# Kernel optimization log

Hardware: AMD Instinct MI355X
Metric: run time of the kernel (lower is better)

The kernel has to match this reference:

```python
import jax, jax.numpy as jnp
import numpy as np

N = 200000   # active voxels
G = 128      # dense grid extent per axis
C = 128      # hidden channels
IN_C = 1
TEMB = 6
K = 27       # 3x3x3 kernel offsets


def _build_neighbors():
    # Sample N unique voxel coordinates in a G^3 grid and build the 27-offset
    # rulebook: neighbor_idx[k, i] = index of voxel at coord[i] + offset[k],
    # or N (sentinel -> zero-padded feature row) if inactive.
    rng = np.random.default_rng(0)
    lin = np.sort(rng.choice(G ** 3, size=N, replace=False)).astype(np.int64)
    x, r = lin // (G * G), lin % (G * G)
    y, z = r // G, r % G
    nidx = np.full((K, N), N, dtype=np.int32)
    k = 0
    for dx in (-1, 0, 1):
        for dy in (-1, 0, 1):
            for dz in (-1, 0, 1):
                nx, ny, nz = x + dx, y + dy, z + dz
                valid = (nx >= 0) & (nx < G) & (ny >= 0) & (ny < G) & (nz >= 0) & (nz < G)
                key = nx * (G * G) + ny * G + nz
                pos = np.searchsorted(lin, key)
                posc = np.clip(pos, 0, N - 1)
                found = valid & (lin[posc] == key)
                nidx[k] = np.where(found, posc, N).astype(np.int32)
                k += 1
    return jnp.asarray(nidx)


def setup_inputs() -> dict:
    key = jax.random.key(0)
    ks = jax.random.split(key, 8)
    s = jnp.float32(0.05)
    return {
        "features": jax.random.normal(ks[0], (N, IN_C), jnp.float32),
        "t": jax.random.randint(ks[1], (N,), 0, 1000, jnp.int32),
        "neighbor_idx": _build_neighbors(),
        "W1": jax.random.normal(ks[2], (K, IN_C + TEMB, C), jnp.float32) * s,
        "b1": jnp.zeros((C,), jnp.float32),
        "W2": jax.random.normal(ks[3], (K, C, C), jnp.float32) * s,
        "b2": jnp.zeros((C,), jnp.float32),
        "W3": jax.random.normal(ks[4], (C, C), jnp.float32) * s,
        "b3": jnp.zeros((C,), jnp.float32),
        "W4": jax.random.normal(ks[5], (C, 1), jnp.float32) * s,
        "b4": jnp.zeros((1,), jnp.float32),
    }


def _sinusoidal(t, dim):
    half = dim // 2
    freqs = (2.0 ** jnp.arange(half, dtype=jnp.float32)) * jnp.pi  # 2^k * pi
    ang = t.astype(jnp.float32)[:, None] * freqs[None, :]
    return jnp.concatenate([jnp.sin(ang), jnp.cos(ang)], -1)  # [N, dim]


def _sparse_conv3(x, W, b, nidx):
    # Submanifold sparse 3x3x3 conv: for each of 27 offsets, gather neighbor
    # features (zero row for missing) and accumulate a [Cin,Cout] matmul.
    xpad = jnp.concatenate([x, jnp.zeros((1, x.shape[1]), x.dtype)], 0)  # sentinel row
    acc0 = jnp.zeros((x.shape[0], W.shape[-1]), x.dtype)

    def step(acc, kw):
        idx, Wk = kw
        return acc + xpad[idx] @ Wk, None

    acc, _ = jax.lax.scan(step, acc0, (nidx, W))
    return acc + b


def reference(features, t, neighbor_idx, W1, b1, W2, b2, W3, b3, W4, b4):
    # time-embedding concat  [N, 1+6]
    x = jnp.concatenate([features, _sinusoidal(t, TEMB)], -1)
    # SparseConv3d(k=3) + Dropout(eval: identity) + SiLU
    h = jax.nn.silu(_sparse_conv3(x, W1, b1, neighbor_idx))
    h = jax.nn.silu(_sparse_conv3(h, W2, b2, neighbor_idx))
    # SparseConv3d(k=1) + SiLU  == pointwise matmul
    h = jax.nn.silu(h @ W3 + b3)
    # final 1x1 conv to out_channels=1
    return h @ W4 + b4
```

## Files before the change

### kernel.cpp

```cpp
#include <hip/hip_runtime.h>
#include <math.h>

#define N_VOX 200000
#define CCH   128
#define KOFF  27

typedef __attribute__((ext_vector_type(8))) short bf16x8;
typedef __attribute__((ext_vector_type(4))) float f32x4;

__device__ __forceinline__ float silu_f(float x) {
    return x / (1.0f + expf(-x));
}
__device__ __forceinline__ unsigned short f2bf(float x) {
    unsigned int u = __float_as_uint(x);
    u = (u + 0x7FFFu + ((u >> 16) & 1u)) >> 16;
    return (unsigned short)u;
}
__device__ __forceinline__ int xcd_swz(int orig, int nwg) {
    int q = nwg >> 3, r = nwg & 7;
    int xcd = orig & 7, pos = orig >> 3;
    return (xcd < r ? xcd * (q + 1) : r * (q + 1) + (xcd - r) * q) + pos;
}
__device__ __forceinline__ void gload_lds16(const void* g, void* l) {
    __builtin_amdgcn_global_load_lds(
        (const __attribute__((address_space(1))) unsigned int*)g,
        (__attribute__((address_space(3))) unsigned int*)l, 16, 0, 0);
}

__global__ void embed_kernel(const float* __restrict__ feat,
                             const int* __restrict__ t,
                             unsigned short* __restrict__ xeb) {
    int i = blockIdx.x * blockDim.x + threadIdx.x;
    if (i > N_VOX) return;
    union { unsigned short u[8]; int4 v; } o;
    if (i == N_VOX) {
        o.v = make_int4(0, 0, 0, 0);
    } else {
        o.u[0] = f2bf(feat[i]);
        float tf = (float)t[i];
#pragma unroll
        for (int kk = 0; kk < 3; ++kk) {
            float freq = (float)M_PI * (float)(1 << kk);
            float ang = tf * freq;
            o.u[1 + kk] = f2bf(sinf(ang));
            o.u[4 + kk] = f2bf(cosf(ang));
        }
        o.u[7] = 0;
    }
    *(int4*)(xeb + (size_t)i * 8) = o.v;
}

__global__ void convert_w1(const float* __restrict__ W1,
                           unsigned short* __restrict__ W1f) {
    int g = blockIdx.x * 256 + threadIdx.x;
    if (g >= 7 * 8 * 64) return;
    int l = g & 63;
    int rest = g >> 6;
    int nf = rest & 7;
    int kk = rest >> 3;
    int o = kk * 4 + (l >> 4);
    int co = nf * 16 + (l & 15);
    union { unsigned short u[8]; int4 v; } out;
#pragma unroll
    for (int j = 0; j < 8; ++j) {
        float w = 0.f;
        if (o < KOFF && j < 7) w = W1[((size_t)o * 7 + j) * CCH + co];
        out.u[j] = f2bf(w);
    }
    *(int4*)(W1f + (size_t)g * 8) = out.v;
}

__global__ void convert_w2(const float* __restrict__ W2,
                           unsigned short* __restrict__ W2f) {
    int g = blockIdx.x * 256 + threadIdx.x;
    int l = g & 63;
    int rest = g >> 6;
    int nf = rest & 7;
    int kkk = rest >> 3;
    int k = kkk >> 2, kk = kkk & 3;
    int ci0 = kk * 32 + (l >> 4) * 8;
    int co = nf * 16 + (l & 15);
    union { unsigned short u[8]; int4 v; } out;
#pragma unroll
    for (int j = 0; j < 8; ++j)
        out.u[j] = f2bf(W2[((size_t)k * CCH + ci0 + j) * CCH + co]);
    *(int4*)(W2f + (size_t)g * 8) = out.v;
}

__global__ void convert_w3(const float* __restrict__ W3,
                           unsigned short* __restrict__ W3f) {
    int g = blockIdx.x * 256 + threadIdx.x;
    if (g >= 4 * 8 * 64) return;
    int l = g & 63;
    int rest = g >> 6;
    int nf = rest & 7;
    int kk = rest >> 3;
    int ci0 = kk * 32 + (l >> 4) * 8;
    int co = nf * 16 + (l & 15);
    union { unsigned short u[8]; int4 v; } out;
#pragma unroll
    for (int j = 0; j < 8; ++j)
        out.u[j] = f2bf(W3[(size_t)(ci0 + j) * CCH + co]);
    *(int4*)(W3f + (size_t)g * 8) = out.v;
}

__global__ __launch_bounds__(256) void conv1_mfma(
    const unsigned short* __restrict__ xeb, const int* __restrict__ nidx,
    const unsigned short* __restrict__ W1f, const float* __restrict__ b1,
    unsigned short* __restrict__ h1b) {
    __shared__ int4 bufmem[2048];
    __shared__ int idxAll[128 * 28];

    int tid = threadIdx.x;
    int l = tid & 63, w = tid >> 6;
    int mw = w >> 1, nwv = w & 1;
    int wg = xcd_swz(blockIdx.x, gridDim.x);
    int v0 = wg * 128;

    for (int g = tid; g < KOFF * 128; g += 256) {
        int k = g >> 7, vi = g & 127;
        int v = v0 + vi;
        idxAll[vi * 28 + k] = (v < N_VOX) ? nidx[(size_t)k * N_VOX + v] : N_VOX;
    }
    if (tid < 128) idxAll[tid * 28 + 27] = N_VOX;
    __syncthreads();

    f32x4 acc[4][4];
#pragma unroll
    for (int m = 0; m < 4; ++m)
#pragma unroll
        for (int n = 0; n < 4; ++n) acc[m][n] = (f32x4)0.f;

    {
        int4 g0[2]; int rr[2], cc[2];
#pragma unroll
        for (int u = 0; u < 2; ++u) {
            int q = u * 256 + tid;
            int r = q >> 2, oo = q & 3;
            int idx = idxAll[r * 28 + oo];
            g0[u] = *(const int4*)(xeb + (size_t)idx * 8);
            rr[u] = r; cc[u] = oo ^ (r & 3);
        }
#pragma unroll
        for (int u = 0; u < 2; ++u) bufmem[rr[u] * 5 + cc[u]] = g0[u];
    }
    __syncthreads();

    for (int kk = 0; kk < 7; ++kk) {
        int cur = kk & 1;
        int4 gg[2]; int rr[2], cc[2];
        if (kk < 6) {
#pragma unroll
            for (int u = 0; u < 2; ++u) {
                int q = u * 256 + tid;
                int r = q >> 2, oo = q & 3;
                int idx = idxAll[r * 28 + (kk + 1) * 4 + oo];
                gg[u] = *(const int4*)(xeb + (size_t)idx * 8);
                rr[u] = r; cc[u] = oo ^ (r & 3);
            }
        }
        bf16x8 a[4], b[4];
#pragma unroll
        for (int n = 0; n < 4; ++n) {
            int nf = nwv * 4 + n;
            b[n] = *(const bf16x8*)(W1f + ((size_t)(kk * 8 + nf) * 64 + l) * 8);
        }
#pragma unroll
        for (int m = 0; m < 4; ++m) {
            int r = mw * 64 + m * 16 + (l & 15);
            int c = l >> 4;
            a[m] = *(const bf16x8*)&bufmem[cur * 640 + r * 5 + (c ^ (r & 3))];
        }
#pragma unroll
        for (int m = 0; m < 4; ++m)
#pragma unroll
            for (int n = 0; n < 4; ++n)
                acc[m][n] = __builtin_amdgcn_mfma_f32_16x16x32_bf16(
                    a[m], b[n], acc[m][n], 0, 0, 0);
        if (kk < 6) {
#pragma unroll
            for (int u = 0; u < 2; ++u)
                bufmem[(cur ^ 1) * 640 + rr[u] * 5 + cc[u]] = gg[u];
        }
        __syncthreads();
    }

    float bias[4];
#pragma unroll
    for (int n = 0; n < 4; ++n) bias[n] = b1[nwv * 64 + n * 16 + (l & 15)];
    unsigned short* H16 = (unsigned short*)bufmem;
#pragma unroll
    for (int m = 0; m < 4; ++m) {
        int rbase = mw * 64 + m * 16 + (l >> 4) * 4;
#pragma unroll
        for (int n = 0; n < 4; ++n) {
            int ch = nwv * 64 + n * 16 + (l & 15);
            int c = ch >> 3;
            f32x4 d = acc[m][n];
#pragma unroll
            for (int ri = 0; ri < 4; ++ri) {
                int r = rbase + ri;
                int s = (c & 8) | ((c & 7) ^ (r & 7));
                H16[r * 128 + s * 8 + (ch & 7)] = f2bf(silu_f(d[ri] + bias[n]));
            }
        }
    }
    __syncthreads();
#pragma unroll
    for (int u = 0; u < 8; ++u) {
        int q = u * 256 + tid;
        int r = q >> 4, s = q & 15;
        int c = (s & 8) | ((s & 7) ^ (r & 7));
        int v = v0 + r;
        if (v < N_VOX)
            *(int4*)(h1b + (size_t)v * CCH + c * 8) = bufmem[r * 16 + s];
    }
    if (blockIdx.x == 0 && tid < 16)
        *(int4*)(h1b + (size_t)N_VOX * CCH + tid * 8) = make_int4(0, 0, 0, 0);
}

#define STAGE_S(buf, sq, ib) {                                             \
    _Pragma("unroll") for (int _u = 0; _u < 8; ++_u) {                     \
        int _q = _u * 256 + tid;                                           \
        int _row = ((_q >> 7) << 4) | (_q & 15);                           \
        int _hi = (_q >> 4) & 3;                                           \
        int _kk = (_q >> 6) & 1;                                           \
        int _idx = idxbuf[ib][_row];                                       \
        gload_lds16((const char*)h1b + ((size_t)(unsigned)_idx << 8) +     \
                        ((sq) & 1) * 128 + _kk * 64 + _hi * 16,            \
                    (void*)&Abuf[buf][_q]);                                \
    }                                                                      \
}

#define LOADB_S(dst, sq) {                                                 \
    const unsigned short* _wb = W2f + (size_t)((sq) >> 1) * 16384 +        \
                                (size_t)((sq) & 1) * 2 * 4096;             \
    _Pragma("unroll") for (int _kk = 0; _kk < 2; ++_kk)                    \
        _Pragma("unroll") for (int _n = 0; _n < 4; ++_n)                   \
            dst[_kk][_n] = *(const bf16x8*)(_wb +                          \
                ((size_t)(_kk * 8 + nwv * 4 + _n) * 64 + l) * 8);          \
}

#define MFMA_S(cur, bfr) {                                                 \
    _Pragma("unroll") for (int _kk = 0; _kk < 2; ++_kk) {                  \
        bf16x8 _a[8];                                                      \
        _Pragma("unroll") for (int _m = 0; _m < 8; ++_m) {                 \
            int _R = mw * 8 + _m;                                          \
            _a[_m] = *(const bf16x8*)&Abuf[cur][((_R * 2 + _kk) << 6) + l];\
        }                                                                  \
        __builtin_amdgcn_s_setprio(1);                                     \
        _Pragma("unroll") for (int _m = 0; _m < 8; ++_m)                   \
            _Pragma("unroll") for (int _n = 0; _n < 4; ++_n)               \
                acc[_m][_n] = __builtin_amdgcn_mfma_f32_16x16x32_bf16(     \
                    _a[_m], bfr[_kk][_n], acc[_m][_n], 0, 0, 0);           \
        __builtin_amdgcn_s_setprio(0);                                     \
    }                                                                      \
}

#define STEP_S(SQ, CUR, DO_STAGE, DO_IDX) {                                \
    bf16x8 bfr[2][4];                                                      \
    LOADB_S(bfr, SQ);                                                      \
    __builtin_amdgcn_sched_barrier(0);                                     \
    if (DO_STAGE) { STAGE_S((CUR) ^ 1, (SQ) + 1, ((((SQ) + 1) >> 1) & 1)); }\
    if (DO_IDX) {                                                          \
        int _k1 = ((SQ) >> 1) + 1;                                         \
        int _v = v0 + tid;                                                 \
        idxbuf[_k1 & 1][tid] =                                             \
            (_v < N_VOX) ? nidx[(size_t)_k1 * N_VOX + _v] : N_VOX;         \
    }                                                                      \
    __builtin_amdgcn_sched_barrier(0);                                     \
    MFMA_S(CUR, bfr);                                                      \
    asm volatile("s_waitcnt vmcnt(0)" ::: "memory");                       \
    __builtin_amdgcn_s_barrier();                                          \
}

__global__ __launch_bounds__(256, 2) void conv2_mfma(
    const unsigned short* __restrict__ h1b, const int* __restrict__ nidx,
    const unsigned short* __restrict__ W2f, const float* __restrict__ b2,
    const unsigned short* __restrict__ W3f, const float* __restrict__ b3,
    const float* __restrict__ W4, const float* __restrict__ b4,
    float* __restrict__ out) {
    __shared__ int4 Abuf[2][2048];
    __shared__ int idxbuf[2][256];
    __shared__ float Osum[512];

    int tid = threadIdx.x;
    int l = tid & 63, w = tid >> 6;
    int mw = w >> 1, nwv = w & 1;
    int wg = xcd_swz(blockIdx.x, gridDim.x);
    int v0 = wg * 256;

    f32x4 acc[8][4];
#pragma unroll
    for (int m = 0; m < 8; ++m)
#pragma unroll
        for (int n = 0; n < 4; ++n) acc[m][n] = (f32x4)0.f;

    {
        int v = v0 + tid;
        idxbuf[0][tid] = (v < N_VOX) ? nidx[v] : N_VOX;
    }
    __syncthreads();
    STAGE_S(0, 0, 0);
    {
        int v = v0 + tid;
        idxbuf[1][tid] = (v < N_VOX) ? nidx[(size_t)N_VOX + v] : N_VOX;
    }
    asm volatile("s_waitcnt vmcnt(0)" ::: "memory");
    __syncthreads();

    for (int sp = 0; sp < 52; sp += 2) {
        STEP_S(sp, 0, true, ((sp >> 1) + 1 < KOFF));
        STEP_S(sp + 1, 1, true, false);
    }
    STEP_S(52, 0, true, false);
    STEP_S(53, 1, false, false);

    float bias2[4];
#pragma unroll
    for (int n = 0; n < 4; ++n) bias2[n] = b2[nwv * 64 + n * 16 + (l & 15)];
    unsigned short* H16 = (unsigned short*)&Abuf[0][0];
#pragma unroll
    for (int m = 0; m < 8; ++m) {
        int rbase = mw * 128 + m * 16 + (l >> 4) * 4;
#pragma unroll
        for (int n = 0; n < 4; ++n) {
            int ch = nwv * 64 + n * 16 + (l & 15);
            int c = ch >> 3;
            f32x4 d = acc[m][n];
#pragma unroll
            for (int ri = 0; ri < 4; ++ri) {
                int r = rbase + ri;
                int s = (c & 8) | ((c & 7) ^ (r & 7));
                H16[r * 128 + s * 8 + (ch & 7)] = f2bf(silu_f(d[ri] + bias2[n]));
            }
        }
    }
    __syncthreads();

    f32x4 p[8][4];
#pragma unroll
    for (int m = 0; m < 8; ++m)
#pragma unroll
        for (int n = 0; n < 4; ++n) p[m][n] = (f32x4)0.f;
#pragma unroll
    for (int kk = 0; kk < 4; ++kk) {
        bf16x8 a[8], b[4];
#pragma unroll
        for (int n = 0; n < 4; ++n) {
            int nf = nwv * 4 + n;
            b[n] = *(const bf16x8*)(W3f + ((size_t)(kk * 8 + nf) * 64 + l) * 8);
        }
#pragma unroll
        for (int m = 0; m < 8; ++m) {
            int r = mw * 128 + m * 16 + (l & 15);
            int c = kk * 4 + (l >> 4);
            int s = (c & 8) | ((c & 7) ^ (r & 7));
            a[m] = *(const bf16x8*)&H16[r * 128 + s * 8];
        }
#pragma unroll
        for (int m = 0; m < 8; ++m)
#pragma unroll
            for (int n = 0; n < 4; ++n)
                p[m][n] = __builtin_amdgcn_mfma_f32_16x16x32_bf16(
                    a[m], b[n], p[m][n], 0, 0, 0);
    }

    float w4v[4], b3v[4];
#pragma unroll
    for (int n = 0; n < 4; ++n) {
        int ch = nwv * 64 + n * 16 + (l & 15);
        w4v[n] = W4[ch];
        b3v[n] = b3[ch];
    }
#pragma unroll
    for (int m = 0; m < 8; ++m) {
        float po[4] = {0.f, 0.f, 0.f, 0.f};
#pragma unroll
        for (int n = 0; n < 4; ++n) {
            f32x4 d = p[m][n];
#pragma unroll
            for (int ri = 0; ri < 4; ++ri)
                po[ri] += silu_f(d[ri] + b3v[n]) * w4v[n];
        }
#pragma unroll
        for (int off = 1; off < 16; off <<= 1)
#pragma unroll
            for (int ri = 0; ri < 4; ++ri)
                po[ri] += __shfl_xor(po[ri], off, 64);
        if ((l & 15) == 0) {
            int rbase = mw * 128 + m * 16 + (l >> 4) * 4;
#pragma unroll
            for (int ri = 0; ri < 4; ++ri)
                Osum[nwv * 256 + rbase + ri] = po[ri];
        }
    }
    __syncthreads();
    {
        int v = v0 + tid;
        if (v < N_VOX) out[v] = Osum[tid] + Osum[256 + tid] + b4[0];
    }
}

extern "C" void kernel_launch(void* const* d_in, const int* in_sizes, int n_in,
                              void* d_out, int out_size, void* d_ws,
                              size_t ws_size, hipStream_t stream) {
    const float* feat = (const float*)d_in[0];
    const int* t      = (const int*)d_in[1];
    const int* nidx   = (const int*)d_in[2];
    const float* W1   = (const float*)d_in[3];
    const float* b1   = (const float*)d_in[4];
    const float* W2   = (const float*)d_in[5];
    const float* b2   = (const float*)d_in[6];
    const float* W3   = (const float*)d_in[7];
    const float* b3   = (const float*)d_in[8];
    const float* W4   = (const float*)d_in[9];
    const float* b4   = (const float*)d_in[10];
    float* out = (float*)d_out;

    char* ws = (char*)d_ws;
    size_t off = 0;
    unsigned short* xeb = (unsigned short*)(ws + off);
    off += ((size_t)(N_VOX + 1) * 8 * 2 + 255) & ~(size_t)255;
    unsigned short* h1b = (unsigned short*)(ws + off);
    off += ((size_t)(N_VOX + 1) * CCH * 2 + 255) & ~(size_t)255;
    unsigned short* W1f = (unsigned short*)(ws + off);
    off += ((size_t)7 * 8 * 64 * 8 * 2 + 255) & ~(size_t)255;
    unsigned short* W2f = (unsigned short*)(ws + off);
    off += ((size_t)(KOFF + 1) * 4 * 8 * 64 * 8 * 2 + 255) & ~(size_t)255;
    unsigned short* W3f = (unsigned short*)(ws + off);

    int grid1 = (N_VOX + 127) / 128;
    int grid2 = (N_VOX + 255) / 256;
    embed_kernel<<<(N_VOX + 1 + 255) / 256, 256, 0, stream>>>(feat, t, xeb);
    convert_w1<<<(7 * 8 * 64 + 255) / 256, 256, 0, stream>>>(W1, W1f);
    convert_w2<<<(KOFF * 4 * 8 * 64) / 256, 256, 0, stream>>>(W2, W2f);
    convert_w3<<<(4 * 8 * 64 + 255) / 256, 256, 0, stream>>>(W3, W3f);
    conv1_mfma<<<grid1, 256, 0, stream>>>(xeb, nidx, W1f, b1, h1b);
    conv2_mfma<<<grid2, 256, 0, stream>>>(h1b, nidx, W2f, b2, W3f, b3, W4, b4, out);
}
```

Measured before the change: 277.3 us.

## Restructure conv2 into 512-thread triple-buffered pipeline with LDS-staged weights

conv2 now runs 512 threads per block (8 waves, 2x4 warp tiling) and uses three LDS buffers holding both gathered activations and W2 slices. Loads go straight to LDS, and each K-half is split into four phases that interleave async gathers with MFMA groups under fine-grained barriers and partial vmcnt waits. Neighbor indices are prefetched into a three-slot ring. The epilogue is reworked so each wave computes a 32-row slice of the W3/W4 head and writes the output directly, with no cross-wave LDS reduction. This is meant to hide gather latency and cut redundant per-wave global weight loads, at the cost of one block per CU and many more barriers.

```diff
diff --git a/kernel.cpp b/kernel.cpp
--- a/kernel.cpp
+++ b/kernel.cpp
@@ -219,113 +219,150 @@
         *(int4*)(h1b + (size_t)N_VOX * CCH + tid * 8) = make_int4(0, 0, 0, 0);
 }
 
-#define STAGE_S(buf, sq, ib) {                                             \
-    _Pragma("unroll") for (int _u = 0; _u < 8; ++_u) {                     \
-        int _q = _u * 256 + tid;                                           \
-        int _row = ((_q >> 7) << 4) | (_q & 15);                           \
-        int _hi = (_q >> 4) & 3;                                           \
-        int _kk = (_q >> 6) & 1;                                           \
-        int _idx = idxbuf[ib][_row];                                       \
-        gload_lds16((const char*)h1b + ((size_t)(unsigned)_idx << 8) +     \
-                        ((sq) & 1) * 128 + _kk * 64 + _hi * 16,            \
-                    (void*)&Abuf[buf][_q]);                                \
-    }                                                                      \
-}
-
-#define LOADB_S(dst, sq) {                                                 \
-    const unsigned short* _wb = W2f + (size_t)((sq) >> 1) * 16384 +        \
-                                (size_t)((sq) & 1) * 2 * 4096;             \
-    _Pragma("unroll") for (int _kk = 0; _kk < 2; ++_kk)                    \
-        _Pragma("unroll") for (int _n = 0; _n < 4; ++_n)                   \
-            dst[_kk][_n] = *(const bf16x8*)(_wb +                          \
-                ((size_t)(_kk * 8 + nwv * 4 + _n) * 64 + l) * 8);          \
-}
-
-#define MFMA_S(cur, bfr) {                                                 \
-    _Pragma("unroll") for (int _kk = 0; _kk < 2; ++_kk) {                  \
-        bf16x8 _a[8];                                                      \
-        _Pragma("unroll") for (int _m = 0; _m < 8; ++_m) {                 \
-            int _R = mw * 8 + _m;                                          \
-            _a[_m] = *(const bf16x8*)&Abuf[cur][((_R * 2 + _kk) << 6) + l];\
-        }                                                                  \
-        __builtin_amdgcn_s_setprio(1);                                     \
-        _Pragma("unroll") for (int _m = 0; _m < 8; ++_m)                   \
-            _Pragma("unroll") for (int _n = 0; _n < 4; ++_n)               \
-                acc[_m][_n] = __builtin_amdgcn_mfma_f32_16x16x32_bf16(     \
-                    _a[_m], bfr[_kk][_n], acc[_m][_n], 0, 0, 0);           \
-        __builtin_amdgcn_s_setprio(0);                                     \
-    }                                                                      \
-}
-
-#define STEP_S(SQ, CUR, DO_STAGE, DO_IDX) {                                \
-    bf16x8 bfr[2][4];                                                      \
-    LOADB_S(bfr, SQ);                                                      \
+#define STG_A(P, s3, h, U) {                                               \
+    int _T = (U) * 8 + w;                                                  \
+    int _r16 = _T >> 1, _kkq = _T & 1;                                     \
+    int _idx = idxL[s3][_r16 * 16 + (l & 15)];                             \
+    gload_lds16((const char*)h1b + ((size_t)(unsigned)_idx << 8) +         \
+                    (h) * 128 + _kkq * 64 + (l >> 4) * 16,                 \
+                (void*)&(P)[(U) * 512 + tid]);                             \
+}
+#define STG_B(P, k2, h, U) {                                               \
+    gload_lds16((const char*)W2f + (size_t)(k2) * 32768 + (h) * 16384 +    \
+                    (size_t)((U) * 512 + tid) * 16,                        \
+                (void*)&(P)[2048 + (U) * 512 + tid]);                      \
+}
+
+#define MFMA8(Q) {                                                         \
+    __builtin_amdgcn_s_setprio(1);                                         \
+    acc[(Q)*2+0][0] = __builtin_amdgcn_mfma_f32_16x16x32_bf16(_a00, bfr[0][0], acc[(Q)*2+0][0], 0, 0, 0); \
+    acc[(Q)*2+0][1] = __builtin_amdgcn_mfma_f32_16x16x32_bf16(_a00, bfr[0][1], acc[(Q)*2+0][1], 0, 0, 0); \
+    acc[(Q)*2+1][0] = __builtin_amdgcn_mfma_f32_16x16x32_bf16(_a10, bfr[0][0], acc[(Q)*2+1][0], 0, 0, 0); \
+    acc[(Q)*2+1][1] = __builtin_amdgcn_mfma_f32_16x16x32_bf16(_a10, bfr[0][1], acc[(Q)*2+1][1], 0, 0, 0); \
+    acc[(Q)*2+0][0] = __builtin_amdgcn_mfma_f32_16x16x32_bf16(_a01, bfr[1][0], acc[(Q)*2+0][0], 0, 0, 0); \
+    acc[(Q)*2+0][1] = __builtin_amdgcn_mfma_f32_16x16x32_bf16(_a01, bfr[1][1], acc[(Q)*2+0][1], 0, 0, 0); \
+    acc[(Q)*2+1][0] = __builtin_amdgcn_mfma_f32_16x16x32_bf16(_a11, bfr[1][0], acc[(Q)*2+1][0], 0, 0, 0); \
+    acc[(Q)*2+1][1] = __builtin_amdgcn_mfma_f32_16x16x32_bf16(_a11, bfr[1][1], acc[(Q)*2+1][1], 0, 0, 0); \
+    __builtin_amdgcn_s_setprio(0);                                         \
+}
+
+#define AREADS(Pc, Q)                                                      \
+    bf16x8 _a00 = *(const bf16x8*)&(Pc)[((mw * 8 + (Q)*2 + 0) * 2 + 0) * 64 + l]; \
+    bf16x8 _a01 = *(const bf16x8*)&(Pc)[((mw * 8 + (Q)*2 + 0) * 2 + 1) * 64 + l]; \
+    bf16x8 _a10 = *(const bf16x8*)&(Pc)[((mw * 8 + (Q)*2 + 1) * 2 + 0) * 64 + l]; \
+    bf16x8 _a11 = *(const bf16x8*)&(Pc)[((mw * 8 + (Q)*2 + 1) * 2 + 1) * 64 + l];
+
+#define PHASE(Pc, Q, STAGE_STMTS) {                                        \
+    AREADS(Pc, Q)                                                          \
+    STAGE_STMTS                                                            \
+    asm volatile("s_barrier" ::: "memory");                                \
+    asm volatile("s_waitcnt lgkmcnt(0)" ::: "memory");                     \
     __builtin_amdgcn_sched_barrier(0);                                     \
-    if (DO_STAGE) { STAGE_S((CUR) ^ 1, (SQ) + 1, ((((SQ) + 1) >> 1) & 1)); }\
-    if (DO_IDX) {                                                          \
-        int _k1 = ((SQ) >> 1) + 1;                                         \
-        int _v = v0 + tid;                                                 \
-        idxbuf[_k1 & 1][tid] =                                             \
-            (_v < N_VOX) ? nidx[(size_t)_k1 * N_VOX + _v] : N_VOX;         \
-    }                                                                      \
+    MFMA8(Q)                                                               \
+    asm volatile("s_barrier" ::: "memory");                                \
+}
+
+#define PHASE_END(Pc, Q, ENDSTMTS) {                                       \
+    AREADS(Pc, Q)                                                          \
+    asm volatile("s_barrier" ::: "memory");                                \
+    asm volatile("s_waitcnt lgkmcnt(0)" ::: "memory");                     \
     __builtin_amdgcn_sched_barrier(0);                                     \
-    MFMA_S(CUR, bfr);                                                      \
-    asm volatile("s_waitcnt vmcnt(0)" ::: "memory");                       \
-    __builtin_amdgcn_s_barrier();                                          \
-}
-
-__global__ __launch_bounds__(256, 2) void conv2_mfma(
+    MFMA8(Q)                                                               \
+    ENDSTMTS                                                               \
+    asm volatile("s_barrier" ::: "memory");                                \
+}
+
+#define RDB(Pc) {                                                          \
+    bfr[0][0] = *(const bf16x8*)&(Pc)[2048 + (0 * 8 + nwv * 2 + 0) * 64 + l]; \
+    bfr[0][1] = *(const bf16x8*)&(Pc)[2048 + (0 * 8 + nwv * 2 + 1) * 64 + l]; \
+    bfr[1][0] = *(const bf16x8*)&(Pc)[2048 + (1 * 8 + nwv * 2 + 0) * 64 + l]; \
+    bfr[1][1] = *(const bf16x8*)&(Pc)[2048 + (1 * 8 + nwv * 2 + 1) * 64 + l]; \
+}
+
+__global__ __launch_bounds__(512, 1) void conv2_mfma(
     const unsigned short* __restrict__ h1b, const int* __restrict__ nidx,
     const unsigned short* __restrict__ W2f, const float* __restrict__ b2,
     const unsigned short* __restrict__ W3f, const float* __restrict__ b3,
     const float* __restrict__ W4, const float* __restrict__ b4,
     float* __restrict__ out) {
-    __shared__ int4 Abuf[2][2048];
-    __shared__ int idxbuf[2][256];
-    __shared__ float Osum[512];
+    __shared__ int4 Pbuf[3][3072];
+    __shared__ int idxL[3][256];
 
     int tid = threadIdx.x;
     int l = tid & 63, w = tid >> 6;
-    int mw = w >> 1, nwv = w & 1;
+    int mw = w >> 2, nwv = w & 3;
     int wg = xcd_swz(blockIdx.x, gridDim.x);
     int v0 = wg * 256;
 
-    f32x4 acc[8][4];
+    for (int g = tid; g < 3 * 256; g += 512) {
+        int k = g >> 8, vi = g & 255;
+        int v = v0 + vi;
+        idxL[k][vi] = (v < N_VOX) ? nidx[(size_t)k * N_VOX + v] : N_VOX;
+    }
+    __syncthreads();
+
+    f32x4 acc[8][2];
 #pragma unroll
     for (int m = 0; m < 8; ++m)
 #pragma unroll
-        for (int n = 0; n < 4; ++n) acc[m][n] = (f32x4)0.f;
-
-    {
-        int v = v0 + tid;
-        idxbuf[0][tid] = (v < N_VOX) ? nidx[v] : N_VOX;
-    }
-    __syncthreads();
-    STAGE_S(0, 0, 0);
-    {
-        int v = v0 + tid;
-        idxbuf[1][tid] = (v < N_VOX) ? nidx[(size_t)N_VOX + v] : N_VOX;
-    }
+        for (int n = 0; n < 2; ++n) acc[m][n] = (f32x4)0.f;
+
+    int4* P0 = Pbuf[0];
+    int4* P1 = Pbuf[1];
+    int4* P2 = Pbuf[2];
+
+    STG_A(P0, 0, 0, 0); STG_A(P0, 0, 0, 1); STG_A(P0, 0, 0, 2); STG_A(P0, 0, 0, 3);
+    STG_B(P0, 0, 0, 0); STG_B(P0, 0, 0, 1);
+    STG_A(P1, 0, 1, 0); STG_A(P1, 0, 1, 1); STG_A(P1, 0, 1, 2); STG_A(P1, 0, 1, 3);
+    STG_B(P1, 0, 1, 0); STG_B(P1, 0, 1, 1);
     asm volatile("s_waitcnt vmcnt(0)" ::: "memory");
     __syncthreads();
 
-    for (int sp = 0; sp < 52; sp += 2) {
-        STEP_S(sp, 0, true, ((sp >> 1) + 1 < KOFF));
-        STEP_S(sp + 1, 1, true, false);
-    }
-    STEP_S(52, 0, true, false);
-    STEP_S(53, 1, false, false);
-
-    float bias2[4];
-#pragma unroll
-    for (int n = 0; n < 4; ++n) bias2[n] = b2[nwv * 64 + n * 16 + (l & 15)];
-    unsigned short* H16 = (unsigned short*)&Abuf[0][0];
+    for (int tp = 0; tp < 27; ++tp) {
+        int s3 = (tp + 1) % 3;
+        int k2 = tp + 1;
+        int knew = tp + 2; if (knew > 26) knew = 26;
+        int slotw = (tp + 2) % 3;
+        int idxreg;
+        {
+            bf16x8 bfr[2][2];
+            RDB(P0);
+            PHASE(P0, 0, {
+                idxreg = nidx[(size_t)knew * N_VOX + v0 + (tid & 255)];
+                STG_A(P2, s3, 0, 0); STG_A(P2, s3, 0, 1);
+            });
+            PHASE(P0, 1, { STG_A(P2, s3, 0, 2); STG_A(P2, s3, 0, 3); });
+            PHASE(P0, 2, { STG_B(P2, k2, 0, 0); STG_B(P2, k2, 0, 1); });
+            PHASE_END(P0, 3, {
+                asm volatile("s_waitcnt vmcnt(7)" ::: "memory");
+            });
+        }
+        {
+            bf16x8 bfr[2][2];
+            RDB(P1);
+            PHASE(P1, 0, { STG_A(P0, s3, 1, 0); STG_A(P0, s3, 1, 1); });
+            PHASE(P1, 1, { STG_A(P0, s3, 1, 2); STG_A(P0, s3, 1, 3); });
+            PHASE(P1, 2, { STG_B(P0, k2, 1, 0); STG_B(P0, k2, 1, 1); });
+            PHASE_END(P1, 3, {
+                asm volatile("s_waitcnt vmcnt(6)" ::: "memory");
+                if (tid < 256) idxL[slotw][tid] = idxreg;
+            });
+        }
+        int4* tmp = P0; P0 = P2; P2 = P1; P1 = tmp;
+    }
+    asm volatile("s_waitcnt vmcnt(0)" ::: "memory");
+    __syncthreads();
+
+    float bias2[2];
+#pragma unroll
+    for (int n = 0; n < 2; ++n) bias2[n] = b2[nwv * 32 + n * 16 + (l & 15)];
+    unsigned short* H16 = (unsigned short*)&Pbuf[0][0];
 #pragma unroll
     for (int m = 0; m < 8; ++m) {
         int rbase = mw * 128 + m * 16 + (l >> 4) * 4;
 #pragma unroll
-        for (int n = 0; n < 4; ++n) {
-            int ch = nwv * 64 + n * 16 + (l & 15);
+        for (int n = 0; n < 2; ++n) {
+            int ch = nwv * 32 + n * 16 + (l & 15);
             int c = ch >> 3;
             f32x4 d = acc[m][n];
 #pragma unroll
@@ -338,50 +375,43 @@
     }
     __syncthreads();
 
-    f32x4 p[8][4];
-#pragma unroll
-    for (int m = 0; m < 8; ++m)
-#pragma unroll
-        for (int n = 0; n < 4; ++n) p[m][n] = (f32x4)0.f;
+    f32x4 p2[2][8];
+#pragma unroll
+    for (int m = 0; m < 2; ++m)
+#pragma unroll
+        for (int n = 0; n < 8; ++n) p2[m][n] = (f32x4)0.f;
 #pragma unroll
     for (int kk = 0; kk < 4; ++kk) {
-        bf16x8 a[8], b[4];
-#pragma unroll
-        for (int n = 0; n < 4; ++n) {
-            int nf = nwv * 4 + n;
-            b[n] = *(const bf16x8*)(W3f + ((size_t)(kk * 8 + nf) * 64 + l) * 8);
-        }
-#pragma unroll
-        for (int m = 0; m < 8; ++m) {
-            int r = mw * 128 + m * 16 + (l & 15);
+        bf16x8 a[2], b[8];
+#pragma unroll
+        for (int n = 0; n < 8; ++n)
+            b[n] = *(const bf16x8*)(W3f + ((size_t)(kk * 8 + n) * 64 + l) * 8);
+#pragma unroll
+        for (int m = 0; m < 2; ++m) {
+            int r = w * 32 + m * 16 + (l & 15);
             int c = kk * 4 + (l >> 4);
             int s = (c & 8) | ((c & 7) ^ (r & 7));
             a[m] = *(const bf16x8*)&H16[r * 128 + s * 8];
         }
 #pragma unroll
-        for (int m = 0; m < 8; ++m)
-#pragma unroll
-            for (int n = 0; n < 4; ++n)
-                p[m][n] = __builtin_amdgcn_mfma_f32_16x16x32_bf16(
-                    a[m], b[n], p[m][n], 0, 0, 0);
-    }
-
-    float w4v[4], b3v[4];
-#pragma unroll
-    for (int n = 0; n < 4; ++n) {
-        int ch = nwv * 64 + n * 16 + (l & 15);
-        w4v[n] = W4[ch];
-        b3v[n] = b3[ch];
-    }
-#pragma unroll
-    for (int m = 0; m < 8; ++m) {
+        for (int m = 0; m < 2; ++m)
+#pragma unroll
+            for (int n = 0; n < 8; ++n)
+                p2[m][n] = __builtin_amdgcn_mfma_f32_16x16x32_bf16(
+                    a[m], b[n], p2[m][n], 0, 0, 0);
+    }
+
+#pragma unroll
+    for (int m = 0; m < 2; ++m) {
         float po[4] = {0.f, 0.f, 0.f, 0.f};
 #pragma unroll
-        for (int n = 0; n < 4; ++n) {
-            f32x4 d = p[m][n];
+        for (int n = 0; n < 8; ++n) {
+            int ch = n * 16 + (l & 15);
+            float b3v = b3[ch], w4v = W4[ch];
+            f32x4 d = p2[m][n];
 #pragma unroll
             for (int ri = 0; ri < 4; ++ri)
-                po[ri] += silu_f(d[ri] + b3v[n]) * w4v[n];
+                po[ri] += silu_f(d[ri] + b3v) * w4v;
         }
 #pragma unroll
         for (int off = 1; off < 16; off <<= 1)
@@ -389,16 +419,13 @@
             for (int ri = 0; ri < 4; ++ri)
                 po[ri] += __shfl_xor(po[ri], off, 64);
         if ((l & 15) == 0) {
-            int rbase = mw * 128 + m * 16 + (l >> 4) * 4;
-#pragma unroll
-            for (int ri = 0; ri < 4; ++ri)
-                Osum[nwv * 256 + rbase + ri] = po[ri];
-        }
-    }
-    __syncthreads();
-    {
-        int v = v0 + tid;
-        if (v < N_VOX) out[v] = Osum[tid] + Osum[256 + tid] + b4[0];
+            int rbase = v0 + w * 32 + m * 16 + (l >> 4) * 4;
+#pragma unroll
+            for (int ri = 0; ri < 4; ++ri) {
+                int v = rbase + ri;
+                if (v < N_VOX) out[v] = po[ri] + b4[0];
+            }
+        }
     }
 }
 
@@ -437,5 +464,5 @@
     convert_w2<<<(KOFF * 4 * 8 * 64) / 256, 256, 0, stream>>>(W2, W2f);
     convert_w3<<<(4 * 8 * 64 + 255) / 256, 256, 0, stream>>>(W3, W3f);
     conv1_mfma<<<grid1, 256, 0, stream>>>(xeb, nidx, W1f, b1, h1b);
-    conv2_mfma<<<grid2, 256, 0, stream>>>(h1b, nidx, W2f, b2, W3f, b3, W4, b4, out);
-}
+    conv2_mfma<<<grid2, 512, 0, stream>>>(h1b, nidx, W2f, b2, W3f, b3, W4, b4, out);
+}
```

New measurement: 378.0 us. 36.3% more time.
